# Kernel optimization log

Hardware: AMD Instinct MI355X
Metric: run time of the kernel (lower is better)

The kernel has to match this reference:

```python
import jax, jax.numpy as jnp
import numpy as np

B, T, Nt = 64, 256, 77      # batch, motion length, text tokens
H, L = 8, 64                # num_heads, latent_dim per head
D = H * L                   # 512 model dim
Pt = 256                    # text_latent_dim
Ht = 1                      # num_text_heads
E, K = 8, 2                 # num_experts, topk
TEMB = 2048                 # time_embed_dim
MAXS, MAXTS = 512, 77       # max_seq_len, max_text_seq_len
NEG = -1e6


def _ln(x, g, b, eps=1e-5):
    m = jnp.mean(x, -1, keepdims=True)
    v = jnp.mean((x - m) ** 2, -1, keepdims=True)
    return (x - m) * jax.lax.rsqrt(v + eps) * g + b


def _gelu(x):
    return jax.nn.gelu(x, approximate=False)


def _moe_tokens(x, gate_w, fc1w, fc1b, fc2w, fc2b):
    # top-k softmax gate (fp32) + expert FFNs; dense compute, sparse combine.
    logits = x.astype(jnp.float32) @ gate_w.astype(jnp.float32)          # [Ntok,E]
    gates = jax.nn.softmax(logits, axis=-1)
    topv, topi = jax.lax.top_k(gates, K)
    topv = topv / jnp.sum(topv, -1, keepdims=True)
    dense = jnp.sum(jax.nn.one_hot(topi, E, dtype=topv.dtype) * topv[..., None], axis=1)
    dense = dense.astype(x.dtype)                                        # [Ntok,E]
    y = jnp.zeros((x.shape[0], fc2w.shape[-1]), x.dtype)
    for e in range(E):  # small fixed expert loop
        h = _gelu(x @ fc1w[e] + fc1b[e])
        y = y + dense[:, e:e + 1] * (h @ fc2w[e] + fc2b[e])
    return y


def _moe_block(x, pos, gate_w, fc1w, fc1b, fc2w, fc2b, projw, projb):
    # x: [B,Tn,Hn,Din]; add learned positional embedding, MoE over tokens, GELU, proj.
    b, t, h, d = x.shape
    x = x + pos[:, :t]
    y = _moe_tokens(x.reshape(-1, d), gate_w, fc1w, fc1b, fc2w, fc2b)
    y = _gelu(y) @ projw + projb
    return y.reshape(b, t, h, -1)


def _fwd(x, xf, emb, src_mask, norm_g, norm_b, tnorm_g, tnorm_b, m_pos, m_gate, m_fc1w, m_fc1b, m_fc2w, m_fc2b, m_projw, m_projb, t_pos, t_gate, t_fc1w, t_fc1b, t_fc2w, t_fc2b, t_projw, t_projb, body_w, sb_embw, sb_embb, sb_ng, sb_nb, sb_outw, sb_outb, cond_type):
    Bx, Tx, Dx = x.shape
    x4 = x.reshape(Bx, Tx, H, L)
    tf = xf.reshape(Bx, Nt, Ht, Pt)
    text_feat = _moe_block(_ln(tf, tnorm_g, tnorm_b), t_pos, t_gate, t_fc1w, t_fc1b, t_fc2w, t_fc2b, t_projw, t_projb)      # [B,Nt,Ht,2L]
    motion_feat = _moe_block(_ln(x4, norm_g, norm_b), m_pos, m_gate, m_fc1w, m_fc1b, m_fc2w, m_fc2b, m_projw, m_projb)      # [B,T,H,4L]
    # static body-part mixing
    bw = jax.nn.softmax(body_w, axis=1)
    body_feat = jnp.einsum('hl,bnld->bnhd', bw, motion_feat[..., :L]).reshape(Bx, Tx, Dx)
    tc = (cond_type % 10 > 0).astype(x.dtype).reshape(Bx, 1, 1, 1)
    sm = src_mask.reshape(Bx, Tx, 1, 1)
    key_text = jnp.broadcast_to(text_feat[..., :L] + (1.0 - tc) * NEG, (Bx, Nt, H, L))
    key_motion = motion_feat[..., L:2 * L] + (1.0 - sm) * NEG
    key = jax.nn.softmax(jnp.concatenate([key_text, key_motion], axis=1), axis=1)  # softmax over N
    val_text = jnp.broadcast_to(text_feat[..., L:] * tc, (Bx, Nt, H, L))
    val_motion = motion_feat[..., 2 * L:3 * L] * sm
    value = jnp.concatenate([val_text, val_motion], axis=1)                        # [B,N,H,L]
    query = jax.nn.softmax(motion_feat[..., 3 * L:], axis=-1)                      # [B,T,H,L]
    attn = jnp.einsum('bnhd,bnhl->bhdl', key, value)                               # [B,H,L,L]
    y_t = jnp.einsum('bnhd,bhdl->bnhl', query, attn).reshape(Bx, Tx, Dx)
    # StylizationBlock (eval: dropout is identity)
    h = _ln(body_feat + y_t, sb_ng, sb_nb)
    eo = jax.nn.silu(emb) @ sb_embw + sb_embb                                      # [B,2D]
    h = h * (1.0 + eo[:, None, :Dx]) + eo[:, None, Dx:]
    h = jax.nn.silu(h) @ sb_outw + sb_outb
    return x + h


def setup_inputs() -> dict:
    ks = iter(jax.random.split(jax.random.key(0), 48))
    nrm = lambda shape, s: jax.random.normal(next(ks), shape, jnp.float32) * s
    return {
        "x": nrm((B, T, D), 1.0),
        "xf": nrm((B, Nt, Pt), 1.0),
        "emb": nrm((B, TEMB), 1.0),
        "src_mask": jnp.ones((B, T, 1), jnp.float32),
        "norm_g": jnp.ones((L,), jnp.float32), "norm_b": jnp.zeros((L,), jnp.float32),
        "tnorm_g": jnp.ones((Pt,), jnp.float32), "tnorm_b": jnp.zeros((Pt,), jnp.float32),
        "m_pos": nrm((1, MAXS, H, L), 0.02),
        "m_gate": nrm((L, E), 0.02),
        "m_fc1w": nrm((E, L, 4 * L), 0.02), "m_fc1b": jnp.zeros((E, 4 * L), jnp.float32),
        "m_fc2w": nrm((E, 4 * L, L), 0.02), "m_fc2b": jnp.zeros((E, L), jnp.float32),
        "m_projw": nrm((L, 4 * L), 0.02), "m_projb": jnp.zeros((4 * L,), jnp.float32),
        "t_pos": nrm((1, MAXTS, Ht, Pt), 0.02),
        "t_gate": nrm((Pt, E), 0.02),
        "t_fc1w": nrm((E, Pt, 4 * Pt), 0.02), "t_fc1b": jnp.zeros((E, 4 * Pt), jnp.float32),
        "t_fc2w": nrm((E, 4 * Pt, Pt), 0.02), "t_fc2b": jnp.zeros((E, Pt), jnp.float32),
        "t_projw": nrm((Pt, 2 * L), 0.02), "t_projb": jnp.zeros((2 * L,), jnp.float32),
        "body_w": nrm((H, H), 1.0),
        "sb_embw": nrm((TEMB, 2 * D), 0.02), "sb_embb": jnp.zeros((2 * D,), jnp.float32),
        "sb_ng": jnp.ones((D,), jnp.float32), "sb_nb": jnp.zeros((D,), jnp.float32),
        "sb_outw": nrm((D, D), 0.02), "sb_outb": jnp.zeros((D,), jnp.float32),
        "cond_type": jax.random.randint(next(ks), (B, 1, 1), 0, 100, jnp.int32),
        "motion_length": T,
        "num_intervals": 1,
    }


def reference(x, xf, emb, src_mask, norm_g, norm_b, tnorm_g, tnorm_b, m_pos, m_gate, m_fc1w, m_fc1b, m_fc2w, m_fc2b, m_projw, m_projb, t_pos, t_gate, t_fc1w, t_fc1b, t_fc2w, t_fc2b, t_projw, t_projb, body_w, sb_embw, sb_embb, sb_ng, sb_nb, sb_outw, sb_outb, cond_type, motion_length, num_intervals):
    # motion_length / num_intervals are unused by the forward math (as in the source).
    return _fwd(x, xf, emb, src_mask, norm_g, norm_b, tnorm_g, tnorm_b, m_pos, m_gate, m_fc1w, m_fc1b, m_fc2w, m_fc2b, m_projw, m_projb, t_pos, t_gate, t_fc1w, t_fc1b, t_fc2w, t_fc2b, t_projw, t_projb, body_w, sb_embw, sb_embb, sb_ng, sb_nb, sb_outw, sb_outb, cond_type)
```

## Files before the change

kernel.cpp:

```cpp
#include <hip/hip_runtime.h>
#include <hip/hip_bf16.h>


typedef __hip_bfloat16 bf16;
typedef unsigned short u16;
typedef unsigned int   u32;
typedef __attribute__((ext_vector_type(8))) short short8;
typedef __attribute__((ext_vector_type(4))) short s16x4;
typedef __attribute__((ext_vector_type(4))) float f32x4;

#define MFMA16(a,b,c) __builtin_amdgcn_mfma_f32_16x16x32_bf16(a,b,c,0,0,0)

__device__ __forceinline__ float b2f(bf16 v){ return __bfloat162float(v); }
__device__ __forceinline__ u16 f2bu(float f){
  union { __hip_bfloat16 hh; u16 us; } cv; cv.hh = __float2bfloat16(f); return cv.us;
}
__device__ __forceinline__ float bu2f(u16 v){ return __uint_as_float(((u32)v)<<16); }

__device__ __forceinline__ float geluf(float x){
  float t = x*x;
  float w = x * fmaf(-0.10294453f, t, -2.3022077f);
  float z = exp2f(w);
  return x * __builtin_amdgcn_rcpf(1.f + z);
}
__device__ __forceinline__ float siluf(float x){
  float z = exp2f(-1.442695f * x);
  return x * __builtin_amdgcn_rcpf(1.f + z);
}

__device__ __forceinline__ float wsum(float v){
#pragma unroll
  for (int o=32;o>0;o>>=1) v += __shfl_xor(v,o,64);
  return v;
}
__device__ __forceinline__ float wmax(float v){
#pragma unroll
  for (int o=32;o>0;o>>=1) v = fmaxf(v, __shfl_xor(v,o,64));
  return v;
}
__device__ __forceinline__ void top2(const float* lg, int& i1, int& i2, float& wA){
  i1 = 0; float v1 = lg[0];
#pragma unroll
  for (int e=1;e<8;e++) if (lg[e] > v1){ v1 = lg[e]; i1 = e; }
  i2 = 0; float v2 = -1e30f;
#pragma unroll
  for (int e=0;e<8;e++) if (e != i1 && lg[e] > v2){ v2 = lg[e]; i2 = e; }
  wA = 1.f/(1.f + expf(v2 - v1));
}

__device__ __forceinline__ float sum2_wave(float x, int b0){
  float s = x, ss = x*x;
  float v = (b0 ? ss : s) + __shfl_xor(b0 ? s : ss, 1, 64);
  v += __shfl_xor(v, 2, 64);
  v += __shfl_xor(v, 4, 64);
  v += __shfl_xor(v, 8, 64);
  v += __shfl_xor(v, 16, 64);
  v += __shfl_xor(v, 32, 64);
  return v;
}

__device__ __forceinline__ float rsum8(const float p[8], int lane){
  int b0 = lane & 1, b1 = lane & 2, b2 = lane & 4;
  float w[4], u[2], v;
#pragma unroll
  for (int j=0;j<4;j++){
    float keep = b0 ? p[2*j+1] : p[2*j];
    float send = b0 ? p[2*j]   : p[2*j+1];
    w[j] = keep + __shfl_xor(send, 1, 64);
  }
#pragma unroll
  for (int i=0;i<2;i++){
    float keep = b1 ? w[2*i+1] : w[2*i];
    float send = b1 ? w[2*i]   : w[2*i+1];
    u[i] = keep + __shfl_xor(send, 2, 64);
  }
  {
    float keep = b2 ? u[1] : u[0];
    float send = b2 ? u[0] : u[1];
    v = keep + __shfl_xor(send, 4, 64);
  }
  v += __shfl_xor(v, 8, 64);
  v += __shfl_xor(v, 16, 64);
  v += __shfl_xor(v, 32, 64);
  return v;
}

__device__ __forceinline__ short8 ld8(const u16* p){
  s16x4 lo = *(const s16x4*)p;
  s16x4 hi = *(const s16x4*)(p + 4);
  short8 r;
  r[0]=lo[0]; r[1]=lo[1]; r[2]=lo[2]; r[3]=lo[3];
  r[4]=hi[0]; r[5]=hi[1]; r[6]=hi[2]; r[7]=hi[3];
  return r;
}

__global__ __launch_bounds__(64) void k_zero(int* cnts){ cnts[threadIdx.x] = 0; }

__global__ __launch_bounds__(64) void k_bw(const float* __restrict__ body_w, float* __restrict__ bwv){
  int t = threadIdx.x;
  if (t < 8){
    float v[8]; float mx = -1e30f;
#pragma unroll
    for (int j=0;j<8;j++){ v[j] = body_w[t*8+j]; mx = fmaxf(mx, v[j]); }
    float s = 0.f;
#pragma unroll
    for (int j=0;j<8;j++){ v[j] = expf(v[j]-mx); s += v[j]; }
#pragma unroll
    for (int j=0;j<8;j++) bwv[t*8+j] = v[j]/s;
  }
}

__global__ __launch_bounds__(256) void k_repack(const float* __restrict__ s, u16* __restrict__ d,
                                                int KC, int N, int total){
  int NT = N >> 4;
  for (int t = blockIdx.x*256 + threadIdx.x; t < total; t += gridDim.x*256){
    int j = t & 7, n = (t>>3) & 15, q = (t>>7) & 3;
    int r2 = t >> 9;
    int kc = r2 % KC; int r3 = r2 / KC;
    int nt = r3 % NT; int e = r3 / NT;
    int k = kc*32 + q*8 + j;
    d[t] = f2bu(s[((size_t)(e*(KC*32) + k))*N + nt*16 + n]);
  }
}

__global__ __launch_bounds__(256) void k_count(const int2* __restrict__ eidx, int n, int* __restrict__ cnt){
  __shared__ int h[8];
  int tid = threadIdx.x;
  if (tid < 8) h[tid] = 0;
  __syncthreads();
  for (int i = blockIdx.x*256 + tid; i < n; i += gridDim.x*256){
    int2 e = eidx[i];
    atomicAdd(&h[e.x], 1); atomicAdd(&h[e.y], 1);
  }
  __syncthreads();
  if (tid < 8) atomicAdd(&cnt[tid], h[tid]);
}

__global__ __launch_bounds__(64) void k_scan(int* cnts){
  if (threadIdx.x == 0){
    int s = 0;
    for (int e=0;e<8;e++){ cnts[16+e] = s; cnts[32+e] = s; s += cnts[e]; }
    s = 0;
    for (int e=0;e<8;e++){ cnts[24+e] = s; cnts[40+e] = s; s += cnts[8+e]; }
  }
}

__global__ __launch_bounds__(256) void k_fill(const int2* __restrict__ eidx, int n,
                                              int* __restrict__ off2, int* __restrict__ alist){
  __shared__ int lc[8], gb[8], lc2[8];
  int tid = threadIdx.x;
  if (tid < 8){ lc[tid] = 0; lc2[tid] = 0; }
  __syncthreads();
  for (int i = blockIdx.x*256 + tid; i < n; i += gridDim.x*256){
    int2 e = eidx[i];
    atomicAdd(&lc[e.x], 1); atomicAdd(&lc[e.y], 1);
  }
  __syncthreads();
  if (tid < 8) gb[tid] = atomicAdd(&off2[tid], lc[tid]);
  __syncthreads();
  for (int i = blockIdx.x*256 + tid; i < n; i += gridDim.x*256){
    int2 e = eidx[i];
    int s0 = atomicAdd(&lc2[e.x], 1); alist[gb[e.x] + s0] = i*2;
    int s1 = atomicAdd(&lc2[e.y], 1); alist[gb[e.y] + s1] = i*2 + 1;
  }
}

__global__ __launch_bounds__(256) void k_text_pre(
    const float* __restrict__ xf, const float* __restrict__ tg, const float* __restrict__ tb,
    const float* __restrict__ tpos, const float* __restrict__ gw,
    u16* __restrict__ xtb, int2* __restrict__ eidxT, float2* __restrict__ ewT){
  int tok = blockIdx.x, tid = threadIdx.x;
  int n = tok % 77;
  __shared__ float redw[32], lgs[8];
  int w = tid >> 6, ln = tid & 63;
  int b0 = tid & 1;
  float xv = xf[tok*256 + tid];
  float v = sum2_wave(xv, b0);
  if (ln < 2) redw[w*2 + ln] = v;
  __syncthreads();
  float mean = (redw[0]+redw[2]+redw[4]+redw[6]) * (1.f/256.f);
  float var  = (redw[1]+redw[3]+redw[5]+redw[7]) * (1.f/256.f) - mean*mean;
  float r = rsqrtf(var + 1e-5f);
  float xn = (xv - mean)*r*tg[tid] + tb[tid] + tpos[n*256 + tid];
  xtb[tok*256 + tid] = f2bu(xn);
  float p[8];
#pragma unroll
  for (int e=0;e<8;e++) p[e] = xn * gw[tid*8 + e];
  float vv = rsum8(p, ln);
  __syncthreads();
  if (ln < 8) redw[w*8 + ln] = vv;
  __syncthreads();
  if (tid < 8) lgs[tid] = redw[tid] + redw[8+tid] + redw[16+tid] + redw[24+tid];
  __syncthreads();
  if (tid == 0){
    int i1, i2; float wA; top2(lgs, i1, i2, wA);
    eidxT[tok] = make_int2(i1, i2);
    ewT[tok] = make_float2(wA, 1.f - wA);
  }
}

__global__ __launch_bounds__(256) void k_motion_pre(
    const float* __restrict__ x, const float* __restrict__ ng, const float* __restrict__ nb,
    const float* __restrict__ mpos, const float* __restrict__ gw,
    u16* __restrict__ xmb, int2* __restrict__ eidxM, float2* __restrict__ ewM){
  int tok = blockIdx.x*4 + (threadIdx.x >> 6);
  int d = threadIdx.x & 63;
  int b0 = d & 1;
  float xv = x[(size_t)tok*64 + d];
  float v = sum2_wave(xv, b0);
  float o = __shfl_xor(v, 1, 64);
  float sf  = b0 ? o : v;
  float ssf = b0 ? v : o;
  float mean = sf * (1.f/64.f);
  float var  = ssf * (1.f/64.f) - mean*mean;
  float r = rsqrtf(var + 1e-5f);
  int h = tok & 7; int t = (tok >> 3) & 255;
  float xn = (xv - mean)*r*ng[d] + nb[d] + mpos[(t*8+h)*64 + d];
  xmb[(size_t)tok*64 + d] = f2bu(xn);
  float p[8];
#pragma unroll
  for (int e=0;e<8;e++) p[e] = xn * gw[d*8 + e];
  float vv = rsum8(p, d);
  float lg[8];
#pragma unroll
  for (int e=0;e<8;e++) lg[e] = __shfl(vv, e, 64);
  if (d == 0){
    int i1, i2; float wA; top2(lg, i1, i2, wA);
    eidxM[tok] = make_int2(i1, i2);
    ewM[tok] = make_float2(wA, 1.f - wA);
  }
}

__global__ __launch_bounds__(256) void k_motion_moe(
    const u16* __restrict__ xmb, const int* __restrict__ alistM, const int* __restrict__ cnts,
    const u16* __restrict__ w1pk, const float* __restrict__ fc1b,
    const u16* __restrict__ w2pk, const float* __restrict__ fc2b,
    u16* __restrict__ ycM){
  int e = blockIdx.y, tile = blockIdx.x, tid = threadIdx.x;
  int cnt = cnts[8+e]; int base = tile*32;
  if (base >= cnt) return;
  int nn = min(32, cnt - base); int off = cnts[24+e];
  __shared__ int toks[32];
  __shared__ u16 xs[32*88];
  __shared__ u16 hT[32*280];
  if (tid < 32) toks[tid] = alistM[off + base + min(tid, nn-1)];
  __syncthreads();
  { int row = tid >> 3, c0 = (tid & 7)*8;
    short8 v = *(const short8*)(xmb + (size_t)(toks[row]>>1)*64 + c0);
    *(short8*)&xs[row*88 + c0] = v; }
  __syncthreads();
  int lane = tid & 63, w = tid >> 6;
  int n = lane & 15, q = lane >> 4;
  int mt = w & 1;
  short8 a0 = *(const short8*)&xs[(mt*16 + n)*88 + q*8];
  short8 a1 = *(const short8*)&xs[(mt*16 + n)*88 + 32 + q*8];
  const short8* b1 = (const short8*)(w1pk + (size_t)e*16384);
#pragma unroll
  for (int i=0;i<8;i++){
    int nt = (w>>1)*8 + i;
    f32x4 acc = {0.f,0.f,0.f,0.f};
    acc = MFMA16(a0, b1[(nt*2+0)*64 + lane], acc);
    acc = MFMA16(a1, b1[(nt*2+1)*64 + lane], acc);
    float bias = fc1b[e*256 + nt*16 + n];
#pragma unroll
    for (int r=0;r<4;r++)
      hT[(mt*16 + q*4 + r)*280 + nt*16 + n] = f2bu(geluf(acc[r] + bias));
  }
  __syncthreads();
  short8 a2[8];
#pragma unroll
  for (int kc=0;kc<8;kc++) a2[kc] = *(const short8*)&hT[(mt*16 + n)*280 + kc*32 + q*8];
  const short8* b2 = (const short8*)(w2pk + (size_t)e*16384);
#pragma unroll
  for (int i=0;i<2;i++){
    int nt = (w>>1)*2 + i;
    f32x4 acc = {0.f,0.f,0.f,0.f};
#pragma unroll
    for (int kc=0;kc<8;kc++) acc = MFMA16(a2[kc], b2[(nt*8+kc)*64 + lane], acc);
    float bias = fc2b[e*64 + nt*16 + n];
#pragma unroll
    for (int r=0;r<4;r++){
      int row = mt*16 + q*4 + r;
      if (row < nn) ycM[(size_t)toks[row]*64 + nt*16 + n] = f2bu(acc[r] + bias);
    }
  }
}

__global__ __launch_bounds__(256) void k_text_moe(
    const u16* __restrict__ xtb, const int* __restrict__ alistT, const int* __restrict__ cnts,
    const u16* __restrict__ w1pk, const float* __restrict__ fc1b,
    const u16* __restrict__ w2pk, const float* __restrict__ fc2b,
    float* __restrict__ ycT){
  int e = blockIdx.y, tile = blockIdx.x, tid = threadIdx.x;
  int cnt = cnts[e]; int base = tile*16;
  if (base >= cnt) return;
  int nn = min(16, cnt - base); int off = cnts[16+e];
  __shared__ int toks[16];
  __shared__ u16 xs[16*280];
  __shared__ u16 hT[16*1048];
  if (tid < 16) toks[tid] = alistT[off + base + min(tid, nn-1)];
  __syncthreads();
  { int row = tid >> 4, c0 = (tid & 15)*16;
    const short8* sp = (const short8*)(xtb + (size_t)(toks[row]>>1)*256 + c0);
    short8 v0 = sp[0], v1 = sp[1];
    *(short8*)&xs[row*280 + c0] = v0;
    *(short8*)&xs[row*280 + c0 + 8] = v1; }
  __syncthreads();
  int lane = tid & 63, w = tid >> 6;
  int n = lane & 15, q = lane >> 4;
  short8 a_[8];
#pragma unroll
  for (int kc=0;kc<8;kc++) a_[kc] = *(const short8*)&xs[n*280 + kc*32 + q*8];
  const short8* b1 = (const short8*)(w1pk + (size_t)e*262144);
#pragma unroll 1
  for (int i=0;i<16;i++){
    int nt = w*16 + i;
    f32x4 acc = {0.f,0.f,0.f,0.f};
#pragma unroll
    for (int kc=0;kc<8;kc++) acc = MFMA16(a_[kc], b1[(nt*8+kc)*64 + lane], acc);
    float bias = fc1b[e*1024 + nt*16 + n];
#pragma unroll
    for (int r=0;r<4;r++)
      hT[(q*4 + r)*1048 + nt*16 + n] = f2bu(geluf(acc[r] + bias));
  }
  __syncthreads();
  const short8* b2 = (const short8*)(w2pk + (size_t)e*262144);
  f32x4 acc[4];
#pragma unroll
  for (int i=0;i<4;i++) acc[i] = (f32x4){0.f,0.f,0.f,0.f};
#pragma unroll 1
  for (int kc=0;kc<32;kc++){
    short8 a = *(const short8*)&hT[n*1048 + kc*32 + q*8];
#pragma unroll
    for (int i=0;i<4;i++){
      int nt = w*4 + i;
      acc[i] = MFMA16(a, b2[(nt*32+kc)*64 + lane], acc[i]);
    }
  }
#pragma unroll
  for (int i=0;i<4;i++){
    int nt = w*4 + i;
    float bias = fc2b[e*256 + nt*16 + n];
#pragma unroll
    for (int r=0;r<4;r++){
      int row = q*4 + r;
      if (row < nn) ycT[(size_t)toks[row]*256 + nt*16 + n] = acc[i][r] + bias;
    }
  }
}

__global__ __launch_bounds__(128) void k_text_combine(
    const float* __restrict__ ycT, const float2* __restrict__ ewT,
    const float* __restrict__ pw, const float* __restrict__ pb,
    float* __restrict__ tfeat){
  int t = blockIdx.x, tid = threadIdx.x;
  __shared__ float gy[256];
  float2 w = ewT[t];
  for (int c=tid; c<256; c+=128){
    float y = w.x*ycT[(size_t)(t*2)*256 + c] + w.y*ycT[(size_t)(t*2+1)*256 + c];
    gy[c] = geluf(y);
  }
  __syncthreads();
  float a = pb[tid];
  for (int k=0;k<256;k++) a += gy[k] * pw[k*128 + tid];
  tfeat[(size_t)t*128 + tid] = a;
}

__global__ __launch_bounds__(256) void k_mproj(
    const u16* __restrict__ ycM, const float2* __restrict__ ewM,
    const u16* __restrict__ wpk, const float* __restrict__ pb,
    u16* __restrict__ mf){
  int t0 = blockIdx.x*32, tid = threadIdx.x;
  __shared__ u16 xs[32*88];
  { int row = tid >> 3, c0 = (tid & 7)*8;
    int tok = t0 + row;
    float2 wgt = ewM[tok];
    short8 v0 = *(const short8*)(ycM + (size_t)(tok*2)*64 + c0);
    short8 v1 = *(const short8*)(ycM + (size_t)(tok*2+1)*64 + c0);
    short8 o;
#pragma unroll
    for (int j=0;j<8;j++)
      o[j] = (short)f2bu(geluf(wgt.x*bu2f((u16)v0[j]) + wgt.y*bu2f((u16)v1[j])));
    *(short8*)&xs[row*88 + c0] = o; }
  __syncthreads();
  int lane = tid & 63, w = tid >> 6;
  int n = lane & 15, q = lane >> 4;
  int mt = w & 1;
  short8 a0 = *(const short8*)&xs[(mt*16 + n)*88 + q*8];
  short8 a1 = *(const short8*)&xs[(mt*16 + n)*88 + 32 + q*8];
  const short8* bp = (const short8*)wpk;
#pragma unroll
  for (int i=0;i<8;i++){
    int nt = (w>>1)*8 + i;
    f32x4 acc = {0.f,0.f,0.f,0.f};
    acc = MFMA16(a0, bp[(nt*2+0)*64 + lane], acc);
    acc = MFMA16(a1, bp[(nt*2+1)*64 + lane], acc);
    float bias = pb[nt*16 + n];
#pragma unroll
    for (int r=0;r<4;r++){
      int tok = t0 + mt*16 + q*4 + r;
      mf[(size_t)tok*256 + nt*16 + n] = f2bu(acc[r] + bias);
    }
  }
}

__global__ __launch_bounds__(256) void k_eo1(const float* __restrict__ emb, const float* __restrict__ ew,
                      float* __restrict__ ep){
  int ct = blockIdx.x & 15;
  int ks = blockIdx.x >> 4;
  int tid = threadIdx.x;
  int k0 = ks*128, c0 = ct*64;
  __shared__ float aS[128*68];
  __shared__ float bS[128*64];
#pragma unroll
  for (int i=0;i<8;i++){
    int idx4 = tid + i*256;
    int b = idx4 >> 5, kq = idx4 & 31;
    f32x4 v = *(const f32x4*)(emb + (size_t)b*2048 + k0 + kq*4);
    aS[(kq*4+0)*68 + b] = siluf(v[0]);
    aS[(kq*4+1)*68 + b] = siluf(v[1]);
    aS[(kq*4+2)*68 + b] = siluf(v[2]);
    aS[(kq*4+3)*68 + b] = siluf(v[3]);
  }
#pragma unroll
  for (int i=0;i<8;i++){
    int idx4 = tid + i*256;
    int kk = idx4 >> 4, cq = idx4 & 15;
    *(f32x4*)&bS[kk*64 + cq*4] = *(const f32x4*)(ew + (size_t)(k0+kk)*1024 + c0 + cq*4);
  }
  __syncthreads();
  int cg = tid & 15, bg = tid >> 4;
  f32x4 acc[4] = {{0.f,0.f,0.f,0.f},{0.f,0.f,0.f,0.f},{0.f,0.f,0.f,0.f},{0.f,0.f,0.f,0.f}};
#pragma unroll 4
  for (int kk=0;kk<128;kk++){
    f32x4 a = *(const f32x4*)&aS[kk*68 + bg*4];
    f32x4 bb = *(const f32x4*)&bS[kk*64 + cg*4];
#pragma unroll
    for (int i=0;i<4;i++){
      acc[i][0] += a[i]*bb[0];
      acc[i][1] += a[i]*bb[1];
      acc[i][2] += a[i]*bb[2];
      acc[i][3] += a[i]*bb[3];
    }
  }
#pragma unroll
  for (int i=0;i<4;i++){
    int b = bg*4 + i;
    *(f32x4*)&ep[((size_t)(ks*64 + b))*1024 + c0 + cg*4] = acc[i];
  }
}

__global__ __launch_bounds__(256) void k_eo2(const float* __restrict__ ep, const float* __restrict__ ebias,
                      float* __restrict__ eo){
  int idx = blockIdx.x*256 + threadIdx.x;
  int c = idx & 1023;
  float s = ebias[c];
#pragma unroll
  for (int ks=0;ks<16;ks++) s += ep[(size_t)ks*65536 + idx];
  eo[idx] = s;
}

#define AT_STRIDE 364
__global__ __launch_bounds__(512) void k_attn(const float* __restrict__ tfeat, const u16* __restrict__ mf,
                       const float* __restrict__ src_mask, const int* __restrict__ cond,
                       u16* __restrict__ attnT){
  int b = blockIdx.x >> 3; int h = blockIdx.x & 7;
  int tid = threadIdx.x; int c = tid & 63; int part = tid >> 6;
  __shared__ u16 ebT[64*AT_STRIDE];
  __shared__ u16 vbT[64*AT_STRIDE];
  __shared__ float colmax[64], colsum[64], red[512];
  float tc = ((cond[b] % 10) > 0) ? 1.f : 0.f;
  float negt = (1.f - tc) * (-1e6f);

  float mx = -1e30f;
  for (int k = 0; k < 11; k++){
    int n0 = part*44 + k*4;
    s16x4 kb4, vb4;
#pragma unroll
    for (int jj = 0; jj < 4; jj++){
      int n = n0 + jj;
      float kv, vv;
      if (n < 77){
        const float* trow = tfeat + (b*77+n)*128;
        kv = trow[c] + negt;
        vv = trow[64 + c] * tc;
      } else if (n < 333){
        int t = n - 77; float smv = src_mask[b*256 + t];
        const u16* mrow = mf + ((size_t)(b*256+t)*8+h)*256;
        kv = bu2f(mrow[64 + c]) + (1.f - smv)*(-1e6f);
        vv = bu2f(mrow[128 + c]) * smv;
      } else { kv = -1e30f; vv = 0.f; }
      kb4[jj] = (short)f2bu(kv);
      vb4[jj] = (short)f2bu(vv);
      mx = fmaxf(mx, kv);
    }
    *(s16x4*)&ebT[c*AT_STRIDE + n0] = kb4;
    *(s16x4*)&vbT[c*AT_STRIDE + n0] = vb4;
  }
  red[tid] = mx; __syncthreads();
  if (part == 0){
    float m = red[c];
#pragma unroll
    for (int p=1;p<8;p++) m = fmaxf(m, red[p*64 + c]);
    colmax[c] = m;
  }
  __syncthreads();
  { int rowc = tid >> 3, j = tid & 7;
    float cm = colmax[rowc];
    float s = 0.f;
    for (int k = 0; k < 11; k++){
      int n0 = (j*11 + k)*4;
      s16x4 v4 = *(const s16x4*)&ebT[rowc*AT_STRIDE + n0];
      float e0 = expf(bu2f((u16)v4[0]) - cm);
      float e1 = expf(bu2f((u16)v4[1]) - cm);
      float e2 = expf(bu2f((u16)v4[2]) - cm);
      float e3 = expf(bu2f((u16)v4[3]) - cm);
      s += (e0+e1) + (e2+e3);
      s16x4 o;
      o[0]=(short)f2bu(e0); o[1]=(short)f2bu(e1); o[2]=(short)f2bu(e2); o[3]=(short)f2bu(e3);
      *(s16x4*)&ebT[rowc*AT_STRIDE + n0] = o;
    }
    red[tid] = s;
  }
  __syncthreads();
  if (tid < 64){
    float t2 = 0.f;
#pragma unroll
    for (int p=0;p<8;p++) t2 += red[tid*8 + p];
    colsum[tid] = t2;
  }
  __syncthreads();
  int lane = tid & 63, w = tid >> 6;
  int n16 = lane & 15, q = lane >> 4;
  int mt = w >> 1;
  int ntb = (w & 1) * 2;
  f32x4 acc0 = {0.f,0.f,0.f,0.f}, acc1 = {0.f,0.f,0.f,0.f};
  const u16* ea = &ebT[(mt*16 + n16)*AT_STRIDE + q*8];
  const u16* v0p = &vbT[(ntb*16 + n16)*AT_STRIDE + q*8];
  const u16* v1p = &vbT[((ntb+1)*16 + n16)*AT_STRIDE + q*8];
#pragma unroll
  for (int kc = 0; kc < 11; kc++){
    short8 a  = ld8(ea  + kc*32);
    short8 b0 = ld8(v0p + kc*32);
    short8 b1 = ld8(v1p + kc*32);
    acc0 = MFMA16(a, b0, acc0);
    acc1 = MFMA16(a, b1, acc1);
  }
  float inv[4];
#pragma unroll
  for (int r=0;r<4;r++) inv[r] = __builtin_amdgcn_rcpf(colsum[mt*16 + q*4 + r]);
  u16* outp = attnT + (size_t)(b*8+h)*4096;
  int d0 = mt*16 + q*4;
  {
    int l = ntb*16 + n16;
    s16x4 o;
#pragma unroll
    for (int r=0;r<4;r++) o[r] = (short)f2bu(acc0[r]*inv[r]);
    *(s16x4*)(outp + l*64 + d0) = o;
  }
  {
    int l = (ntb+1)*16 + n16;
    s16x4 o;
#pragma unroll
    for (int r=0;r<4;r++) o[r] = (short)f2bu(acc1[r]*inv[r]);
    *(s16x4*)(outp + l*64 + d0) = o;
  }
}

__global__ __launch_bounds__(256) void k_qs(const u16* __restrict__ mf, u16* __restrict__ qs){
  int tok = blockIdx.x*4 + (threadIdx.x >> 6);
  int d = threadIdx.x & 63;
  float v = bu2f(mf[(size_t)tok*256 + 192 + d]);
  float mx = wmax(v);
  float e = expf(v - mx);
  float s = wsum(e);
  qs[(size_t)tok*64 + d] = f2bu(e/s);
}

__global__ __launch_bounds__(256) void k_yt(const u16* __restrict__ qs, const u16* __restrict__ attnT,
                                            u16* __restrict__ yt){
  int b = blockIdx.x >> 3; int h = blockIdx.x & 7;
  int tid = threadIdx.x;
  int lane = tid & 63, w = tid >> 6;
  int n = lane & 15, q = lane >> 4;
  const u16* qsb = qs + ((size_t)(b*256)*8 + h)*64;
  const u16* ab  = attnT + (size_t)(b*8+h)*4096;
  f32x4 acc[4][4];
#pragma unroll
  for (int mt=0;mt<4;mt++)
#pragma unroll
    for (int nt=0;nt<4;nt++) acc[mt][nt] = (f32x4){0.f,0.f,0.f,0.f};
#pragma unroll
  for (int kc=0;kc<2;kc++){
    short8 a_[4], b_[4];
#pragma unroll
    for (int mt=0;mt<4;mt++){
      int t = w*64 + mt*16 + n;
      a_[mt] = *(const short8*)(qsb + (size_t)t*512 + kc*32 + q*8);
    }
#pragma unroll
    for (int nt=0;nt<4;nt++){
      int l = nt*16 + n;
      b_[nt] = *(const short8*)(ab + l*64 + kc*32 + q*8);
    }
#pragma unroll
    for (int mt=0;mt<4;mt++)
#pragma unroll
      for (int nt=0;nt<4;nt++)
        acc[mt][nt] = MFMA16(a_[mt], b_[nt], acc[mt][nt]);
  }
#pragma unroll
  for (int mt=0;mt<4;mt++)
#pragma unroll
    for (int nt=0;nt<4;nt++){
      int l = nt*16 + n;
#pragma unroll
      for (int r=0;r<4;r++){
        int t = w*64 + mt*16 + q*4 + r;
        yt[((size_t)(b*256+t)*8 + h)*64 + l] = f2bu(acc[mt][nt][r]);
      }
    }
}

__global__ __launch_bounds__(256) void k_j2(const u16* __restrict__ mf, const u16* __restrict__ yt,
                     const float* __restrict__ bwv, const float* __restrict__ eo,
                     const float* __restrict__ sb_ng, const float* __restrict__ sb_nb,
                     float* __restrict__ sbuf){
  int blk = blockIdx.x; int b = blk >> 8; int t = blk & 255;
  int tid = threadIdx.x;
  __shared__ float mfl[512], red[4];
#pragma unroll
  for (int ii=0; ii<2; ii++){
    int idx = tid + ii*256; int h = idx >> 6; int dd = idx & 63;
    mfl[idx] = bu2f(mf[((size_t)(b*256+t)*8+h)*256 + dd]);
  }
  __syncthreads();
  int w = tid >> 6, ln = tid & 63;
  float out[2];
#pragma unroll
  for (int ii=0; ii<2; ii++){
    int idx = tid + ii*256; int h = idx >> 6; int l = idx & 63;
    float a = bu2f(yt[((size_t)(b*256+t)*8 + h)*64 + l]);
    float bs = 0.f;
#pragma unroll
    for (int lh=0; lh<8; lh++) bs += bwv[h*8 + lh] * mfl[lh*64 + l];
    out[ii] = a + bs;
  }
  float psum = wsum(out[0] + out[1]);
  if (ln == 0) red[w] = psum;
  __syncthreads();
  float mean = (red[0]+red[1]+red[2]+red[3]) * (1.f/512.f);
  __syncthreads();
  float c0 = out[0]-mean, c1 = out[1]-mean;
  float pv = wsum(c0*c0 + c1*c1);
  if (ln == 0) red[w] = pv;
  __syncthreads();
  float var = (red[0]+red[1]+red[2]+red[3]) * (1.f/512.f);
  float r = rsqrtf(var + 1e-5f);
#pragma unroll
  for (int ii=0; ii<2; ii++){
    int c = tid + ii*256;
    float hn = (out[ii]-mean)*r*sb_ng[c] + sb_nb[c];
    float e1 = eo[b*1024 + c], e2 = eo[b*1024 + 512 + c];
    float hm = hn*(1.f + e1) + e2;
    sbuf[(size_t)blk*512 + c] = siluf(hm);
  }
}

__global__ __launch_bounds__(256) void k_out(const u16* __restrict__ wpk,
                      const float* __restrict__ bias, const float* __restrict__ x,
                      float* __restrict__ out){
  int r0 = blockIdx.x*32, tid = threadIdx.x;
  __shared__ u16 xs[32*536];
  { int row = tid >> 3, c0 = (tid & 7)*64;
    const f32x4* sp = (const f32x4*)(out + (size_t)(r0+row)*512 + c0);
#pragma unroll
    for (int j=0;j<8;j++){
      f32x4 va = sp[2*j], vb = sp[2*j+1];
      short8 o;
      o[0]=(short)f2bu(va[0]); o[1]=(short)f2bu(va[1]); o[2]=(short)f2bu(va[2]); o[3]=(short)f2bu(va[3]);
      o[4]=(short)f2bu(vb[0]); o[5]=(short)f2bu(vb[1]); o[6]=(short)f2bu(vb[2]); o[7]=(short)f2bu(vb[3]);
      *(short8*)&xs[row*536 + c0 + 8*j] = o;
    } }
  __syncthreads();
  int lane = tid & 63, w = tid >> 6;
  int n = lane & 15, q = lane >> 4;
  int mt = w & 1;
  short8 a_[16];
#pragma unroll
  for (int kc=0;kc<16;kc++) a_[kc] = *(const short8*)&xs[(mt*16 + n)*536 + kc*32 + q*8];
  const short8* bp = (const short8*)wpk;
#pragma unroll 1
  for (int i=0;i<16;i++){
    int nt = (w>>1)*16 + i;
    f32x4 acc = {0.f,0.f,0.f,0.f};
#pragma unroll
    for (int kc=0;kc<16;kc++) acc = MFMA16(a_[kc], bp[(nt*16+kc)*64 + lane], acc);
    int col = nt*16 + n;
    float bv = bias[col];
#pragma unroll
    for (int r=0;r<4;r++){
      size_t rowg = (size_t)(r0 + mt*16 + q*4 + r);
      out[rowg*512 + col] = acc[r] + bv + x[rowg*512 + col];
    }
  }
}

extern "C" void kernel_launch(void* const* d_in, const int* in_sizes, int n_in,
                              void* d_out, int out_size, void* d_ws, size_t ws_size,
                              hipStream_t stream) {
  (void)in_sizes; (void)n_in; (void)out_size; (void)ws_size;
  const float* x        = (const float*)d_in[0];
  const float* xf       = (const float*)d_in[1];
  const float* emb      = (const float*)d_in[2];
  const float* src_mask = (const float*)d_in[3];
  const float* norm_g   = (const float*)d_in[4];
  const float* norm_b   = (const float*)d_in[5];
  const float* tnorm_g  = (const float*)d_in[6];
  const float* tnorm_b  = (const float*)d_in[7];
  const float* m_pos    = (const float*)d_in[8];
  const float* m_gate   = (const float*)d_in[9];
  const float* m_fc1w   = (const float*)d_in[10];
  const float* m_fc1b   = (const float*)d_in[11];
  const float* m_fc2w   = (const float*)d_in[12];
  const float* m_fc2b   = (const float*)d_in[13];
  const float* m_projw  = (const float*)d_in[14];
  const float* m_projb  = (const float*)d_in[15];
  const float* t_pos    = (const float*)d_in[16];
  const float* t_gate   = (const float*)d_in[17];
  const float* t_fc1w   = (const float*)d_in[18];
  const float* t_fc1b   = (const float*)d_in[19];
  const float* t_fc2w   = (const float*)d_in[20];
  const float* t_fc2b   = (const float*)d_in[21];
  const float* t_projw  = (const float*)d_in[22];
  const float* t_projb  = (const float*)d_in[23];
  const float* body_w   = (const float*)d_in[24];
  const float* sb_embw  = (const float*)d_in[25];
  const float* sb_embb  = (const float*)d_in[26];
  const float* sb_ng    = (const float*)d_in[27];
  const float* sb_nb    = (const float*)d_in[28];
  const float* sb_outw  = (const float*)d_in[29];
  const float* sb_outb  = (const float*)d_in[30];
  const int*   cond     = (const int*)d_in[31];

  char* base = (char*)d_ws;
  size_t o = 0;
  auto alloc = [&](size_t bytes)->char*{ char* r = base + o; o += (bytes + 255) & ~(size_t)255; return r; };
  u16*  mf      = (u16*)alloc(67108864);
  char* R       = alloc(33554432);
  float* ep     = (float*)(R);
  u16*  xtb     = (u16*)(R);
  float* ycT    = (float*)(R + 4194304);
  u16*  ycM     = (u16*)(R);
  u16*  attnT   = (u16*)(R);
  u16*  yt      = (u16*)(R + 8388608);
  u16*  xmb     = (u16*)alloc(16777216);
  u16*  qs      = xmb;
  u16*  t1pk    = (u16*)alloc(4194304);
  u16*  t2pk    = (u16*)alloc(4194304);
  u16*  m1pk    = (u16*)alloc(262144);
  u16*  m2pk    = (u16*)alloc(262144);
  u16*  mppk    = (u16*)alloc(32768);
  u16*  wopk    = (u16*)alloc(524288);
  int2* eidxT   = (int2*)alloc(39424);
  float2* ewT   = (float2*)alloc(39424);
  int2* eidxM   = (int2*)alloc(1048576);
  float2* ewM   = (float2*)alloc(1048576);
  int*  alistT  = (int*)alloc(39424);
  int*  alistM  = (int*)alloc(1048576);
  int*  cnts    = (int*)alloc(256);
  float* tfeat  = (float*)alloc(2523136);
  float* eo     = (float*)alloc(262144);
  float* bwv    = (float*)alloc(256);
  float* sbuf   = (float*)d_out;

  k_zero<<<1, 64, 0, stream>>>(cnts);
  k_bw<<<1, 64, 0, stream>>>(body_w, bwv);
  k_repack<<<512, 256, 0, stream>>>(t_fc1w, t1pk, 8, 1024, 2097152);
  k_repack<<<512, 256, 0, stream>>>(t_fc2w, t2pk, 32, 256, 2097152);
  k_repack<<<64, 256, 0, stream>>>(m_fc1w, m1pk, 2, 256, 131072);
  k_repack<<<64, 256, 0, stream>>>(m_fc2w, m2pk, 8, 64, 131072);
  k_repack<<<8, 256, 0, stream>>>(m_projw, mppk, 2, 256, 16384);
  k_repack<<<128, 256, 0, stream>>>(sb_outw, wopk, 16, 512, 262144);
  k_eo1<<<256, 256, 0, stream>>>(emb, sb_embw, ep);
  k_eo2<<<256, 256, 0, stream>>>(ep, sb_embb, eo);

  k_text_pre<<<4928, 256, 0, stream>>>(xf, tnorm_g, tnorm_b, t_pos, t_gate, xtb, eidxT, ewT);
  k_motion_pre<<<32768, 256, 0, stream>>>(x, norm_g, norm_b, m_pos, m_gate, xmb, eidxM, ewM);
  k_count<<<32, 256, 0, stream>>>(eidxT, 4928, cnts);
  k_count<<<256, 256, 0, stream>>>(eidxM, 131072, cnts + 8);
  k_scan<<<1, 64, 0, stream>>>(cnts);
  k_fill<<<32, 256, 0, stream>>>(eidxT, 4928, cnts + 32, alistT);
  k_fill<<<256, 256, 0, stream>>>(eidxM, 131072, cnts + 40, alistM);

  k_text_moe<<<dim3(308, 8), 256, 0, stream>>>(xtb, alistT, cnts, t1pk, t_fc1b, t2pk, t_fc2b, ycT);
  k_text_combine<<<4928, 128, 0, stream>>>(ycT, ewT, t_projw, t_projb, tfeat);

  k_motion_moe<<<dim3(4096, 8), 256, 0, stream>>>(xmb, alistM, cnts, m1pk, m_fc1b, m2pk, m_fc2b, ycM);
  k_mproj<<<4096, 256, 0, stream>>>(ycM, ewM, mppk, m_projb, mf);

  k_qs<<<32768, 256, 0, stream>>>(mf, qs);
  k_attn<<<512, 512, 0, stream>>>(tfeat, mf, src_mask, cond, attnT);
  k_yt<<<512, 256, 0, stream>>>(qs, attnT, yt);
  k_j2<<<16384, 256, 0, stream>>>(mf, yt, bwv, eo, sb_ng, sb_nb, sbuf);
  k_out<<<512, 256, 0, stream>>>(wopk, sb_outb, x, (float*)d_out);
}
```

Measured before the change: 542.1 us.

## Swap MFMA operands and give each wave its own 16-token tile in motion MoE and proj

The motion MoE and motion projection kernels now give each wavefront its own independent 16-token tile. Weights are fed as the A operand and tokens as the B operand, so each lane holds four consecutive output columns of one token. That allows 4-wide vector stores and vector bias loads, and tokens are read straight from global memory without shared-memory staging or block barriers. The MoE hidden activations use a per-wave LDS buffer, and the projection grid is halved to match 64 tokens per block. The aim is less synchronization and LDS traffic and wider stores, at the cost of more weight fragment loads per wave.

```diff
diff --git a/kernel.cpp b/kernel.cpp
--- a/kernel.cpp
+++ b/kernel.cpp
@@ -236,52 +236,48 @@
     const u16* __restrict__ w1pk, const float* __restrict__ fc1b,
     const u16* __restrict__ w2pk, const float* __restrict__ fc2b,
     u16* __restrict__ ycM){
-  int e = blockIdx.y, tile = blockIdx.x, tid = threadIdx.x;
-  int cnt = cnts[8+e]; int base = tile*32;
+  int e = blockIdx.y;
+  int cnt = cnts[8+e];
+  if (blockIdx.x*64 >= cnt) return;
+  int tid = threadIdx.x, w = tid >> 6, lane = tid & 63;
+  int base = (blockIdx.x*4 + w)*16;
+  __shared__ u16 hTs[4][16*264];
   if (base >= cnt) return;
-  int nn = min(32, cnt - base); int off = cnts[24+e];
-  __shared__ int toks[32];
-  __shared__ u16 xs[32*88];
-  __shared__ u16 hT[32*280];
-  if (tid < 32) toks[tid] = alistM[off + base + min(tid, nn-1)];
-  __syncthreads();
-  { int row = tid >> 3, c0 = (tid & 7)*8;
-    short8 v = *(const short8*)(xmb + (size_t)(toks[row]>>1)*64 + c0);
-    *(short8*)&xs[row*88 + c0] = v; }
-  __syncthreads();
-  int lane = tid & 63, w = tid >> 6;
-  int n = lane & 15, q = lane >> 4;
-  int mt = w & 1;
-  short8 a0 = *(const short8*)&xs[(mt*16 + n)*88 + q*8];
-  short8 a1 = *(const short8*)&xs[(mt*16 + n)*88 + 32 + q*8];
+  int nn = min(16, cnt - base);
+  int off = cnts[24+e];
+  u16* hT = hTs[w];
+  int n16 = lane & 15, q = lane >> 4;
+  int slot = alistM[off + base + min(n16, nn-1)];
+  int tok = slot >> 1;
+  short8 x0 = *(const short8*)(xmb + (size_t)tok*64 + q*8);
+  short8 x1 = *(const short8*)(xmb + (size_t)tok*64 + 32 + q*8);
   const short8* b1 = (const short8*)(w1pk + (size_t)e*16384);
 #pragma unroll
-  for (int i=0;i<8;i++){
-    int nt = (w>>1)*8 + i;
+  for (int i=0;i<16;i++){
     f32x4 acc = {0.f,0.f,0.f,0.f};
-    acc = MFMA16(a0, b1[(nt*2+0)*64 + lane], acc);
-    acc = MFMA16(a1, b1[(nt*2+1)*64 + lane], acc);
-    float bias = fc1b[e*256 + nt*16 + n];
-#pragma unroll
-    for (int r=0;r<4;r++)
-      hT[(mt*16 + q*4 + r)*280 + nt*16 + n] = f2bu(geluf(acc[r] + bias));
-  }
-  __syncthreads();
+    acc = MFMA16(b1[(i*2+0)*64 + lane], x0, acc);
+    acc = MFMA16(b1[(i*2+1)*64 + lane], x1, acc);
+    f32x4 bias = *(const f32x4*)(fc1b + e*256 + i*16 + q*4);
+    s16x4 o;
+#pragma unroll
+    for (int r=0;r<4;r++) o[r] = (short)f2bu(geluf(acc[r] + bias[r]));
+    *(s16x4*)&hT[n16*264 + i*16 + q*4] = o;
+  }
   short8 a2[8];
 #pragma unroll
-  for (int kc=0;kc<8;kc++) a2[kc] = *(const short8*)&hT[(mt*16 + n)*280 + kc*32 + q*8];
+  for (int kc=0;kc<8;kc++) a2[kc] = ld8(&hT[n16*264 + kc*32 + q*8]);
   const short8* b2 = (const short8*)(w2pk + (size_t)e*16384);
 #pragma unroll
-  for (int i=0;i<2;i++){
-    int nt = (w>>1)*2 + i;
+  for (int nt=0;nt<4;nt++){
     f32x4 acc = {0.f,0.f,0.f,0.f};
 #pragma unroll
-    for (int kc=0;kc<8;kc++) acc = MFMA16(a2[kc], b2[(nt*8+kc)*64 + lane], acc);
-    float bias = fc2b[e*64 + nt*16 + n];
-#pragma unroll
-    for (int r=0;r<4;r++){
-      int row = mt*16 + q*4 + r;
-      if (row < nn) ycM[(size_t)toks[row]*64 + nt*16 + n] = f2bu(acc[r] + bias);
+    for (int kc=0;kc<8;kc++) acc = MFMA16(b2[(nt*8+kc)*64 + lane], a2[kc], acc);
+    f32x4 bias = *(const f32x4*)(fc2b + e*64 + nt*16 + q*4);
+    if (n16 < nn){
+      s16x4 o;
+#pragma unroll
+      for (int r=0;r<4;r++) o[r] = (short)f2bu(acc[r] + bias[r]);
+      *(s16x4*)(ycM + (size_t)slot*64 + nt*16 + q*4) = o;
     }
   }
 }
@@ -370,37 +366,32 @@
     const u16* __restrict__ ycM, const float2* __restrict__ ewM,
     const u16* __restrict__ wpk, const float* __restrict__ pb,
     u16* __restrict__ mf){
-  int t0 = blockIdx.x*32, tid = threadIdx.x;
-  __shared__ u16 xs[32*88];
-  { int row = tid >> 3, c0 = (tid & 7)*8;
-    int tok = t0 + row;
-    float2 wgt = ewM[tok];
-    short8 v0 = *(const short8*)(ycM + (size_t)(tok*2)*64 + c0);
-    short8 v1 = *(const short8*)(ycM + (size_t)(tok*2+1)*64 + c0);
+  int tid = threadIdx.x, w = tid >> 6, lane = tid & 63;
+  int n16 = lane & 15, q = lane >> 4;
+  int tok = (blockIdx.x*4 + w)*16 + n16;
+  float2 wgt = ewM[tok];
+  short8 bx[2];
+#pragma unroll
+  for (int kc=0;kc<2;kc++){
+    short8 v0 = *(const short8*)(ycM + (size_t)(tok*2)*64 + kc*32 + q*8);
+    short8 v1 = *(const short8*)(ycM + (size_t)(tok*2+1)*64 + kc*32 + q*8);
     short8 o;
 #pragma unroll
     for (int j=0;j<8;j++)
       o[j] = (short)f2bu(geluf(wgt.x*bu2f((u16)v0[j]) + wgt.y*bu2f((u16)v1[j])));
-    *(short8*)&xs[row*88 + c0] = o; }
-  __syncthreads();
-  int lane = tid & 63, w = tid >> 6;
-  int n = lane & 15, q = lane >> 4;
-  int mt = w & 1;
-  short8 a0 = *(const short8*)&xs[(mt*16 + n)*88 + q*8];
-  short8 a1 = *(const short8*)&xs[(mt*16 + n)*88 + 32 + q*8];
+    bx[kc] = o;
+  }
   const short8* bp = (const short8*)wpk;
 #pragma unroll
-  for (int i=0;i<8;i++){
-    int nt = (w>>1)*8 + i;
+  for (int i=0;i<16;i++){
     f32x4 acc = {0.f,0.f,0.f,0.f};
-    acc = MFMA16(a0, bp[(nt*2+0)*64 + lane], acc);
-    acc = MFMA16(a1, bp[(nt*2+1)*64 + lane], acc);
-    float bias = pb[nt*16 + n];
-#pragma unroll
-    for (int r=0;r<4;r++){
-      int tok = t0 + mt*16 + q*4 + r;
-      mf[(size_t)tok*256 + nt*16 + n] = f2bu(acc[r] + bias);
-    }
+    acc = MFMA16(bp[(i*2+0)*64 + lane], bx[0], acc);
+    acc = MFMA16(bp[(i*2+1)*64 + lane], bx[1], acc);
+    f32x4 bias = *(const f32x4*)(pb + i*16 + q*4);
+    s16x4 o;
+#pragma unroll
+    for (int r=0;r<4;r++) o[r] = (short)f2bu(acc[r] + bias[r]);
+    *(s16x4*)(mf + (size_t)tok*256 + i*16 + q*4) = o;
   }
 }
 
@@ -797,7 +788,7 @@
   k_text_combine<<<4928, 128, 0, stream>>>(ycT, ewT, t_projw, t_projb, tfeat);
 
   k_motion_moe<<<dim3(4096, 8), 256, 0, stream>>>(xmb, alistM, cnts, m1pk, m_fc1b, m2pk, m_fc2b, ycM);
-  k_mproj<<<4096, 256, 0, stream>>>(ycM, ewM, mppk, m_projb, mf);
+  k_mproj<<<2048, 256, 0, stream>>>(ycM, ewM, mppk, m_projb, mf);
 
   k_qs<<<32768, 256, 0, stream>>>(mf, qs);
   k_attn<<<512, 512, 0, stream>>>(tfeat, mf, src_mask, cond, attnT);
```

Measured after the change: 558.3 us. +3.0%, slower.
